# Optimization experiments

Measured on AMD Instinct MI355X. Metric: run time of the kernel, lower is better.

## Reference

```python
import jax, jax.numpy as jnp
import numpy as np

QMIN = 0.0
QMAX = 255.0  # uint8, asymmetric


def fake_quant(x, scale, zp):
    # asymmetric uint8 fake-quantization: q = clamp(round(x/s + zp), 0, 255); dq = (q - zp) * s
    s = scale.reshape(())
    z = zp.reshape(())
    q = jnp.clip(jnp.round(x / s + z), QMIN, QMAX)
    return (q - z) * s


def setup_inputs() -> dict:
    key = jax.random.key(0)
    k1, k2 = jax.random.split(key)
    B, M, K, N = 4, 2048, 4096, 4096
    x1 = jax.random.normal(k1, (B, M, K), dtype=jnp.float32)
    x2 = jax.random.normal(k2, (B, K, N), dtype=jnp.float32)
    # realistic learned per-tensor scale / zero-point for ~N(0,1) data over uint8 range
    x1_scale = jnp.full((1,), 8.0 / 255.0, dtype=jnp.float32)
    x1_zp = jnp.full((1,), 128.0, dtype=jnp.float32)
    x2_scale = jnp.full((1,), 8.0 / 255.0, dtype=jnp.float32)
    x2_zp = jnp.full((1,), 128.0, dtype=jnp.float32)
    return {"x1": x1, "x2": x2, "x1_scale": x1_scale, "x1_zp": x1_zp,
            "x2_scale": x2_scale, "x2_zp": x2_zp}


def reference(x1, x2, x1_scale, x1_zp, x2_scale, x2_zp):
    q1 = fake_quant(x1, x1_scale, x1_zp)  # [B, M, K]
    q2 = fake_quant(x2, x2_scale, x2_zp)  # [B, K, N]
    return jnp.matmul(q1, q2)             # [B, M, N]
```

## Files before the change

kernel.cpp:

```cpp
#include <hip/hip_runtime.h>
#include <stdint.h>

typedef int v4i __attribute__((ext_vector_type(4)));

#define GLOBAL_AS __attribute__((address_space(1)))
#define LDS_AS __attribute__((address_space(3)))

__device__ __forceinline__ int quant1(float x, float s, float z, int zi) {
    float q = rintf(x / s + z);
    q = fminf(fmaxf(q, 0.0f), 255.0f);
    return (int)q - zi;
}

__device__ __forceinline__ unsigned qpack4(float4 v, float s, float z, int zi) {
    unsigned q0 = (unsigned)(quant1(v.x, s, z, zi) & 255);
    unsigned q1 = (unsigned)(quant1(v.y, s, z, zi) & 255);
    unsigned q2 = (unsigned)(quant1(v.z, s, z, zi) & 255);
    unsigned q3 = (unsigned)(quant1(v.w, s, z, zi) & 255);
    return q0 | (q1 << 8) | (q2 << 16) | (q3 << 24);
}

__global__ __launch_bounds__(256) void quant_lin(const float* __restrict__ x,
                                                 int8_t* __restrict__ out,
                                                 const float* __restrict__ sp,
                                                 const float* __restrict__ zp,
                                                 long n16) {
    float s = sp[0], z = zp[0];
    int zi = (int)rintf(z);
    long i = (long)blockIdx.x * 256 + threadIdx.x;
    if (i >= n16) return;
    const float4* xv = (const float4*)x;
    uint4 w;
    w.x = qpack4(xv[i * 4 + 0], s, z, zi);
    w.y = qpack4(xv[i * 4 + 1], s, z, zi);
    w.z = qpack4(xv[i * 4 + 2], s, z, zi);
    w.w = qpack4(xv[i * 4 + 3], s, z, zi);
    ((uint4*)out)[i] = w;
}

__global__ __launch_bounds__(256) void quant_bt(const float* __restrict__ x,
                                                int8_t* __restrict__ out,
                                                const float* __restrict__ sp,
                                                const float* __restrict__ zp) {
    constexpr int K = 4096, N = 4096;
    float s = sp[0], z = zp[0];
    int zi = (int)rintf(z);
    size_t bin = (size_t)blockIdx.z * K * N;
    int tid = threadIdx.x;
    int bk = tid >> 4;
    int bn = tid & 15;
    int k0 = blockIdx.y * 64, n0 = blockIdx.x * 64;
    __shared__ unsigned lds[64][17];
    unsigned o0 = 0, o1 = 0, o2 = 0, o3 = 0;
#pragma unroll
    for (int r = 0; r < 4; ++r) {
        float4 v = *(const float4*)(x + bin + (size_t)(k0 + bk * 4 + r) * N + n0 + bn * 4);
        o0 |= (unsigned)(quant1(v.x, s, z, zi) & 255) << (r * 8);
        o1 |= (unsigned)(quant1(v.y, s, z, zi) & 255) << (r * 8);
        o2 |= (unsigned)(quant1(v.z, s, z, zi) & 255) << (r * 8);
        o3 |= (unsigned)(quant1(v.w, s, z, zi) & 255) << (r * 8);
    }
    lds[bn * 4 + 0][bk] = o0;
    lds[bn * 4 + 1][bk] = o1;
    lds[bn * 4 + 2][bk] = o2;
    lds[bn * 4 + 3][bk] = o3;
    __syncthreads();
    int nl = tid >> 2, ch = tid & 3;
    uint4 w;
    w.x = lds[nl][ch * 4 + 0];
    w.y = lds[nl][ch * 4 + 1];
    w.z = lds[nl][ch * 4 + 2];
    w.w = lds[nl][ch * 4 + 3];
    *(uint4*)(out + bin + (size_t)(n0 + nl) * K + k0 + ch * 16) = w;
}

__global__ __launch_bounds__(256, 1) void gemm_i8(const int8_t* __restrict__ A,
                                                  const int8_t* __restrict__ Bt,
                                                  float* __restrict__ C,
                                                  const float* __restrict__ sp1,
                                                  const float* __restrict__ sp2) {
    constexpr int M = 2048, N = 4096, K = 4096;
    constexpr int BM = 256, BN = 256;
    constexpr int NBN = N / BN;

    extern __shared__ char smem[];

    int b = blockIdx.z;
    const int8_t* Ab = A + (size_t)b * M * K;
    const int8_t* Bb = Bt + (size_t)b * N * K;
    float* Cb = C + (size_t)b * M * N;

    int nwg = gridDim.x;
    int wg = blockIdx.x;
    wg = (wg & 7) * (nwg >> 3) + (wg >> 3);
    int by = wg / NBN, bx = wg % NBN;
    int m0 = by * BM, n0 = bx * BN;

    int tid = threadIdx.x;
    int lane = tid & 63, wid = tid >> 6;
    int wr = wid >> 1, wc = wid & 1;
    int l15 = lane & 15, cb = lane >> 4;

    const int8_t* Abase = Ab + (size_t)m0 * K;
    const int8_t* Bbase = Bb + (size_t)n0 * K;

    int r0 = tid >> 2, cc0 = tid & 3;
    int sw0 = cc0 ^ ((r0 >> 1) & 3);
    const size_t JR = (size_t)64 * K;
    const int8_t* pA = Abase + (size_t)r0 * K + sw0 * 16;
    const int8_t* pB = Bbase + (size_t)r0 * K + sw0 * 16;
    const unsigned dbase = (unsigned)tid * 16;

    int aoff[8], boff[8];
#pragma unroll
    for (int m = 0; m < 8; ++m) {
        int r = wr * 128 + m * 16 + l15;
        aoff[m] = r * 64 + ((cb ^ ((r >> 1) & 3)) * 16);
    }
#pragma unroll
    for (int n = 0; n < 8; ++n) {
        int r = wc * 128 + n * 16 + l15;
        boff[n] = 16384 + r * 64 + ((cb ^ ((r >> 1) & 3)) * 16);
    }

    v4i zero = {0, 0, 0, 0};
    v4i acc[8][8];
#pragma unroll
    for (int m = 0; m < 8; ++m)
#pragma unroll
        for (int n = 0; n < 8; ++n) acc[m][n] = zero;

    v4i a0[8], b0[8], a1[8], b1[8];

#define ISSUE(S)                                                                        \
    {                                                                                   \
        char* da = smem + (S)*32768 + dbase;                                            \
        _Pragma("unroll") for (int j = 0; j < 4; ++j)                                   \
            __builtin_amdgcn_global_load_lds((const GLOBAL_AS void*)(pA + j * JR),      \
                                             (LDS_AS void*)(da + j * 4096), 16, 0, 0);  \
        char* db = smem + (S)*32768 + 16384 + dbase;                                    \
        _Pragma("unroll") for (int j = 0; j < 4; ++j)                                   \
            __builtin_amdgcn_global_load_lds((const GLOBAL_AS void*)(pB + j * JR),      \
                                             (LDS_AS void*)(db + j * 4096), 16, 0, 0);  \
        pA += 64;                                                                       \
        pB += 64;                                                                       \
    }

#define RD(S, fa, fb)                                                                   \
    {                                                                                   \
        const char* rb = smem + (S)*32768;                                              \
        _Pragma("unroll") for (int n = 0; n < 8; ++n)                                   \
            fb[n] = *(const v4i*)(rb + boff[n]);                                        \
        _Pragma("unroll") for (int m = 0; m < 8; ++m)                                   \
            fa[m] = *(const v4i*)(rb + aoff[m]);                                        \
    }

#define MM(fa, fb)                                                                      \
    _Pragma("unroll") for (int m = 0; m < 8; ++m)                                       \
        _Pragma("unroll") for (int n = 0; n < 8; ++n)                                   \
            acc[m][n] = __builtin_amdgcn_mfma_i32_16x16x64_i8(fa[m], fb[n],             \
                                                              acc[m][n], 0, 0, 0);

#define WAITBAR(NW)                                                                     \
    asm volatile("s_waitcnt vmcnt(" #NW ")" ::: "memory");                              \
    __builtin_amdgcn_s_barrier();                                                       \
    asm volatile("" ::: "memory");

    ISSUE(0);
    ISSUE(1);
    ISSUE(2);
    WAITBAR(8)
    RD(0, a0, b0);

    for (int it = 0; it < 15; ++it) {
        ISSUE(3); RD(1, a1, b1); MM(a0, b0) WAITBAR(8)
        ISSUE(0); RD(2, a0, b0); MM(a1, b1) WAITBAR(8)
        ISSUE(1); RD(3, a1, b1); MM(a0, b0) WAITBAR(8)
        ISSUE(2); RD(0, a0, b0); MM(a1, b1) WAITBAR(8)
    }
    ISSUE(3); RD(1, a1, b1); MM(a0, b0) WAITBAR(8)
    RD(2, a0, b0); MM(a1, b1) WAITBAR(0)
    RD(3, a1, b1); MM(a0, b0)
    MM(a1, b1)

    float sc = sp1[0] * sp2[0];
    int rr = cb * 4;
#pragma unroll
    for (int m = 0; m < 8; ++m) {
#pragma unroll
        for (int n = 0; n < 8; ++n) {
            float* p = Cb + (size_t)(m0 + wr * 128 + m * 16 + rr) * N +
                       (n0 + wc * 128 + n * 16 + l15);
#pragma unroll
            for (int r = 0; r < 4; ++r) p[(size_t)r * N] = sc * (float)acc[m][n][r];
        }
    }
#undef ISSUE
#undef RD
#undef MM
#undef WAITBAR
}

extern "C" void kernel_launch(void* const* d_in, const int* in_sizes, int n_in,
                              void* d_out, int out_size, void* d_ws, size_t ws_size,
                              hipStream_t stream) {
    const float* x1 = (const float*)d_in[0];
    const float* x2 = (const float*)d_in[1];
    const float* s1 = (const float*)d_in[2];
    const float* z1 = (const float*)d_in[3];
    const float* s2 = (const float*)d_in[4];
    const float* z2 = (const float*)d_in[5];
    float* out = (float*)d_out;

    const int B = 4, M = 2048, K = 4096, N = 4096;
    const size_t ASZ = (size_t)B * M * K;
    const size_t BSZ = (size_t)B * K * N;
    dim3 blk(256);

    static int lds_attr_set = 0;
    if (!lds_attr_set) {
        (void)hipFuncSetAttribute((const void*)gemm_i8,
                                  hipFuncAttributeMaxDynamicSharedMemorySize, 131072);
        lds_attr_set = 1;
    }

    if (ws_size >= ASZ + BSZ) {
        int8_t* Aq = (int8_t*)d_ws;
        int8_t* Bq = Aq + ASZ;
        long n16 = (long)(ASZ / 16);
        quant_lin<<<dim3((unsigned)(n16 / 256)), blk, 0, stream>>>(x1, Aq, s1, z1, n16);
        quant_bt<<<dim3(N / 64, K / 64, B), blk, 0, stream>>>(x2, Bq, s2, z2);
        gemm_i8<<<dim3((M / 256) * (N / 256), 1, B), dim3(256), 131072, stream>>>(
            Aq, Bq, out, s1, s2);
    } else {
        const size_t AB = (size_t)M * K, BB = (size_t)K * N;
        int8_t* Aq = (int8_t*)d_ws;
        int8_t* Bq = Aq + AB;
        for (int b = 0; b < B; ++b) {
            long n16 = (long)(AB / 16);
            quant_lin<<<dim3((unsigned)(n16 / 256)), blk, 0, stream>>>(x1 + (size_t)b * AB, Aq, s1, z1, n16);
            quant_bt<<<dim3(N / 64, K / 64, 1), blk, 0, stream>>>(x2 + (size_t)b * BB, Bq, s2, z2);
            gemm_i8<<<dim3((M / 256) * (N / 256), 1, 1), dim3(256), 131072, stream>>>(
                Aq, Bq, out + (size_t)b * M * N, s1, s2);
        }
    }
}
```

Before: 269.6 us.

## Use 8 waves per GEMM block with MFMA priority and scheduling barriers

Doubles the GEMM workgroup from 4 to 8 waves, with each wave owning a 128x64 sub-tile instead of 128x128. This halves the accumulator registers per wave and spreads the global-to-LDS loads across more threads. It also raises wave priority around the MFMA blocks and adds sched_group_barrier hints to interleave LDS reads with MFMAs. The trade-off is more LDS fragment reads per MFMA (the A fragments are now re-read by four waves instead of two) and more barrier participants.

```diff
diff --git a/kernel.cpp b/kernel.cpp
--- a/kernel.cpp
+++ b/kernel.cpp
@@ -74,13 +74,13 @@
     *(uint4*)(out + bin + (size_t)(n0 + nl) * K + k0 + ch * 16) = w;
 }
 
-__global__ __launch_bounds__(256, 1) void gemm_i8(const int8_t* __restrict__ A,
+__global__ __launch_bounds__(512, 1) void gemm_i8(const int8_t* __restrict__ A,
                                                   const int8_t* __restrict__ Bt,
                                                   float* __restrict__ C,
                                                   const float* __restrict__ sp1,
                                                   const float* __restrict__ sp2) {
     constexpr int M = 2048, N = 4096, K = 4096;
-    constexpr int BM = 256, BN = 256;
+    constexpr int BM = 256, BN = 256, BK = 64;
     constexpr int NBN = N / BN;
 
     extern __shared__ char smem[];
@@ -98,99 +98,114 @@
 
     int tid = threadIdx.x;
     int lane = tid & 63, wid = tid >> 6;
-    int wr = wid >> 1, wc = wid & 1;
+    int wr = wid >> 2, wc = wid & 3;
     int l15 = lane & 15, cb = lane >> 4;
 
-    const int8_t* Abase = Ab + (size_t)m0 * K;
-    const int8_t* Bbase = Bb + (size_t)n0 * K;
-
-    int r0 = tid >> 2, cc0 = tid & 3;
-    int sw0 = cc0 ^ ((r0 >> 1) & 3);
-    const size_t JR = (size_t)64 * K;
-    const int8_t* pA = Abase + (size_t)r0 * K + sw0 * 16;
-    const int8_t* pB = Bbase + (size_t)r0 * K + sw0 * 16;
+    int row0 = tid >> 2, cc0 = tid & 3;
+    int sw0 = cc0 ^ ((row0 >> 1) & 3);
+    const size_t PSTEP = (size_t)128 * K;
+    const int8_t* pA = Ab + (size_t)(m0 + row0) * K + sw0 * 16;
+    const int8_t* pB = Bb + (size_t)(n0 + row0) * K + sw0 * 16;
     const unsigned dbase = (unsigned)tid * 16;
 
-    int aoff[8], boff[8];
-#pragma unroll
-    for (int m = 0; m < 8; ++m) {
-        int r = wr * 128 + m * 16 + l15;
-        aoff[m] = r * 64 + ((cb ^ ((r >> 1) & 3)) * 16);
-    }
-#pragma unroll
-    for (int n = 0; n < 8; ++n) {
-        int r = wc * 128 + n * 16 + l15;
-        boff[n] = 16384 + r * 64 + ((cb ^ ((r >> 1) & 3)) * 16);
-    }
+    int ra = wr * 128 + l15;
+    int aoff0 = ra * 64 + ((cb ^ ((ra >> 1) & 3)) * 16);
+    int rb_ = wc * 64 + l15;
+    int boff0 = 16384 + rb_ * 64 + ((cb ^ ((rb_ >> 1) & 3)) * 16);
 
     v4i zero = {0, 0, 0, 0};
-    v4i acc[8][8];
+    v4i acc[8][4];
 #pragma unroll
     for (int m = 0; m < 8; ++m)
 #pragma unroll
-        for (int n = 0; n < 8; ++n) acc[m][n] = zero;
-
-    v4i a0[8], b0[8], a1[8], b1[8];
+        for (int n = 0; n < 4; ++n) acc[m][n] = zero;
+
+    v4i fA0[8], fB0[4], fA1[8], fB1[4];
 
 #define ISSUE(S)                                                                        \
     {                                                                                   \
-        char* da = smem + (S)*32768 + dbase;                                            \
-        _Pragma("unroll") for (int j = 0; j < 4; ++j)                                   \
-            __builtin_amdgcn_global_load_lds((const GLOBAL_AS void*)(pA + j * JR),      \
-                                             (LDS_AS void*)(da + j * 4096), 16, 0, 0);  \
-        char* db = smem + (S)*32768 + 16384 + dbase;                                    \
-        _Pragma("unroll") for (int j = 0; j < 4; ++j)                                   \
-            __builtin_amdgcn_global_load_lds((const GLOBAL_AS void*)(pB + j * JR),      \
-                                             (LDS_AS void*)(db + j * 4096), 16, 0, 0);  \
-        pA += 64;                                                                       \
-        pB += 64;                                                                       \
+        char* d = smem + (S)*32768 + dbase;                                             \
+        __builtin_amdgcn_global_load_lds((const GLOBAL_AS void*)pA,                     \
+                                         (LDS_AS void*)d, 16, 0, 0);                    \
+        __builtin_amdgcn_global_load_lds((const GLOBAL_AS void*)(pA + PSTEP),           \
+                                         (LDS_AS void*)(d + 8192), 16, 0, 0);           \
+        __builtin_amdgcn_global_load_lds((const GLOBAL_AS void*)pB,                     \
+                                         (LDS_AS void*)(d + 16384), 16, 0, 0);          \
+        __builtin_amdgcn_global_load_lds((const GLOBAL_AS void*)(pB + PSTEP),           \
+                                         (LDS_AS void*)(d + 24576), 16, 0, 0);          \
+        pA += BK;                                                                       \
+        pB += BK;                                                                       \
     }
 
 #define RD(S, fa, fb)                                                                   \
     {                                                                                   \
-        const char* rb = smem + (S)*32768;                                              \
-        _Pragma("unroll") for (int n = 0; n < 8; ++n)                                   \
-            fb[n] = *(const v4i*)(rb + boff[n]);                                        \
+        const char* rbp = smem + (S)*32768;                                             \
+        _Pragma("unroll") for (int n = 0; n < 4; ++n)                                   \
+            fb[n] = *(const v4i*)(rbp + boff0 + n * 1024);                              \
         _Pragma("unroll") for (int m = 0; m < 8; ++m)                                   \
-            fa[m] = *(const v4i*)(rb + aoff[m]);                                        \
+            fa[m] = *(const v4i*)(rbp + aoff0 + m * 1024);                              \
     }
 
 #define MM(fa, fb)                                                                      \
-    _Pragma("unroll") for (int m = 0; m < 8; ++m)                                       \
-        _Pragma("unroll") for (int n = 0; n < 8; ++n)                                   \
-            acc[m][n] = __builtin_amdgcn_mfma_i32_16x16x64_i8(fa[m], fb[n],             \
-                                                              acc[m][n], 0, 0, 0);
-
-#define WAITBAR(NW)                                                                     \
-    asm volatile("s_waitcnt vmcnt(" #NW ")" ::: "memory");                              \
-    __builtin_amdgcn_s_barrier();                                                       \
-    asm volatile("" ::: "memory");
+    {                                                                                   \
+        __builtin_amdgcn_s_setprio(1);                                                  \
+        _Pragma("unroll") for (int m = 0; m < 8; ++m)                                   \
+            _Pragma("unroll") for (int n = 0; n < 4; ++n)                               \
+                acc[m][n] = __builtin_amdgcn_mfma_i32_16x16x64_i8(fa[m], fb[n],         \
+                                                                  acc[m][n], 0, 0, 0);  \
+        __builtin_amdgcn_s_setprio(0);                                                  \
+    }
+
+#define SGB3()                                                                          \
+    __builtin_amdgcn_sched_group_barrier(0x30, 4, 0);                                   \
+    __builtin_amdgcn_sched_group_barrier(0x100, 12, 0);                                 \
+    __builtin_amdgcn_sched_group_barrier(0x8, 32, 0);
+
+#define STEP(SI, SR, CA, CB, NA, NB)                                                    \
+    {                                                                                   \
+        ISSUE(SI);                                                                      \
+        RD(SR, NA, NB);                                                                 \
+        MM(CA, CB);                                                                     \
+        SGB3();                                                                         \
+        asm volatile("s_waitcnt vmcnt(4)" ::: "memory");                                \
+        __builtin_amdgcn_s_barrier();                                                   \
+        asm volatile("" ::: "memory");                                                  \
+    }
 
     ISSUE(0);
     ISSUE(1);
     ISSUE(2);
-    WAITBAR(8)
-    RD(0, a0, b0);
+    asm volatile("s_waitcnt vmcnt(4)" ::: "memory");
+    __builtin_amdgcn_s_barrier();
+    asm volatile("" ::: "memory");
+    RD(0, fA0, fB0);
 
     for (int it = 0; it < 15; ++it) {
-        ISSUE(3); RD(1, a1, b1); MM(a0, b0) WAITBAR(8)
-        ISSUE(0); RD(2, a0, b0); MM(a1, b1) WAITBAR(8)
-        ISSUE(1); RD(3, a1, b1); MM(a0, b0) WAITBAR(8)
-        ISSUE(2); RD(0, a0, b0); MM(a1, b1) WAITBAR(8)
-    }
-    ISSUE(3); RD(1, a1, b1); MM(a0, b0) WAITBAR(8)
-    RD(2, a0, b0); MM(a1, b1) WAITBAR(0)
-    RD(3, a1, b1); MM(a0, b0)
-    MM(a1, b1)
+        STEP(3, 1, fA0, fB0, fA1, fB1)
+        STEP(0, 2, fA1, fB1, fA0, fB0)
+        STEP(1, 3, fA0, fB0, fA1, fB1)
+        STEP(2, 0, fA1, fB1, fA0, fB0)
+    }
+    STEP(3, 1, fA0, fB0, fA1, fB1)
+    {
+        RD(2, fA0, fB0);
+        MM(fA1, fB1);
+        asm volatile("s_waitcnt vmcnt(0)" ::: "memory");
+        __builtin_amdgcn_s_barrier();
+        asm volatile("" ::: "memory");
+    }
+    RD(3, fA1, fB1);
+    MM(fA0, fB0);
+    MM(fA1, fB1);
 
     float sc = sp1[0] * sp2[0];
-    int rr = cb * 4;
+    int r0 = cb * 4;
 #pragma unroll
     for (int m = 0; m < 8; ++m) {
 #pragma unroll
-        for (int n = 0; n < 8; ++n) {
-            float* p = Cb + (size_t)(m0 + wr * 128 + m * 16 + rr) * N +
-                       (n0 + wc * 128 + n * 16 + l15);
+        for (int n = 0; n < 4; ++n) {
+            float* p = Cb + (size_t)(m0 + wr * 128 + m * 16 + r0) * N +
+                       (n0 + wc * 64 + n * 16 + l15);
 #pragma unroll
             for (int r = 0; r < 4; ++r) p[(size_t)r * N] = sc * (float)acc[m][n][r];
         }
@@ -198,7 +213,8 @@
 #undef ISSUE
 #undef RD
 #undef MM
-#undef WAITBAR
+#undef SGB3
+#undef STEP
 }
 
 extern "C" void kernel_launch(void* const* d_in, const int* in_sizes, int n_in,
@@ -230,7 +246,7 @@
         long n16 = (long)(ASZ / 16);
         quant_lin<<<dim3((unsigned)(n16 / 256)), blk, 0, stream>>>(x1, Aq, s1, z1, n16);
         quant_bt<<<dim3(N / 64, K / 64, B), blk, 0, stream>>>(x2, Bq, s2, z2);
-        gemm_i8<<<dim3((M / 256) * (N / 256), 1, B), dim3(256), 131072, stream>>>(
+        gemm_i8<<<dim3((M / 256) * (N / 256), 1, B), dim3(512), 131072, stream>>>(
             Aq, Bq, out, s1, s2);
     } else {
         const size_t AB = (size_t)M * K, BB = (size_t)K * N;
@@ -240,7 +256,7 @@
             long n16 = (long)(AB / 16);
             quant_lin<<<dim3((unsigned)(n16 / 256)), blk, 0, stream>>>(x1 + (size_t)b * AB, Aq, s1, z1, n16);
             quant_bt<<<dim3(N / 64, K / 64, 1), blk, 0, stream>>>(x2 + (size_t)b * BB, Bq, s2, z2);
-            gemm_i8<<<dim3((M / 256) * (N / 256), 1, 1), dim3(256), 131072, stream>>>(
+            gemm_i8<<<dim3((M / 256) * (N / 256), 1, 1), dim3(512), 131072, stream>>>(
                 Aq, Bq, out + (size_t)b * M * N, s1, s2);
         }
     }
```

New measurement: 250.2 us (median of 3 runs). 7.2% less time.
